# Optimization experiments

Measured on AMD Instinct MI355X. Metric: run time of the kernel, lower is better.

Reference implementation:

```python
import jax, jax.numpy as jnp
import numpy as np

N_NODES = 100000


def _gcn_conv(x, W, b, src, dst, num_nodes):
    """PyG-style GCNConv: add self-loops, symmetric normalization, linear.
    x: [N, Fin], W: [Fin, Fout], b: [Fout], src/dst: [E] (already include self-loops).
    """
    h = x @ W  # [N, Fout] transform first (PyG order), keeps edge traffic at Fout width
    ones = jnp.ones(dst.shape[0], dtype=h.dtype)
    deg = jax.ops.segment_sum(ones, dst, num_segments=num_nodes)  # degree of A+I
    dinv = jnp.where(deg > 0, jax.lax.rsqrt(deg), 0.0)
    norm = dinv[src] * dinv[dst]  # [E]
    msg = h[src] * norm[:, None]  # [E, Fout] gather + scale
    out = jax.ops.segment_sum(msg, dst, num_segments=num_nodes)  # scatter-add
    return out + b


def setup_inputs() -> dict:
    key = jax.random.key(0)
    k1, k2, k3, k4, k5 = jax.random.split(key, 5)
    input_dim, hidden_dim, embedding_dim = 128, 64, 32
    x = jax.random.normal(k1, (N_NODES, input_dim), dtype=jnp.float32)
    edge_index = jax.random.randint(k2, (2, 1600000), 0, N_NODES, dtype=jnp.int32)
    # Glorot-like init for weights
    W1 = jax.random.normal(k3, (input_dim, hidden_dim), dtype=jnp.float32) / np.sqrt(input_dim)
    b1 = jnp.zeros((hidden_dim,), dtype=jnp.float32)
    W2 = jax.random.normal(k4, (hidden_dim, embedding_dim), dtype=jnp.float32) / np.sqrt(hidden_dim)
    b2 = jnp.zeros((embedding_dim,), dtype=jnp.float32)
    return {"x": x, "edge_index": edge_index, "W1": W1, "b1": b1, "W2": W2, "b2": b2}


def reference(x, edge_index, W1, b1, W2, b2):
    num_nodes = x.shape[0]
    loop = jnp.arange(num_nodes, dtype=edge_index.dtype)
    src = jnp.concatenate([edge_index[0], loop])  # add self-loops (PyG default)
    dst = jnp.concatenate([edge_index[1], loop])
    h = _gcn_conv(x, W1, b1, src, dst, num_nodes)
    h = jax.nn.relu(h)
    z = _gcn_conv(h, W2, b2, src, dst, num_nodes)
    return z
```

## Files before the change

kernel.cpp:

```cpp
#include <hip/hip_runtime.h>
#include <hip/hip_bf16.h>


#define MAXBUCK 512

typedef unsigned int uint32;

__device__ __forceinline__ void fma4(float4& a, float s, const float4& w) {
    a.x = fmaf(s, w.x, a.x); a.y = fmaf(s, w.y, a.y);
    a.z = fmaf(s, w.z, a.z); a.w = fmaf(s, w.w, a.w);
}
__device__ __forceinline__ uint32 bf16rn(float f) {
    uint32 u = __float_as_uint(f);
    return (u + 0x7fffu + ((u >> 16) & 1u)) >> 16;
}
__device__ __forceinline__ float bflo(uint32 v) { return __uint_as_float(v << 16); }
__device__ __forceinline__ float bfhi(uint32 v) { return __uint_as_float(v & 0xffff0000u); }

__global__ void k_initcur(int* __restrict__ cursor, int nbuck, int cap) {
    int i = blockIdx.x * blockDim.x + threadIdx.x;
    if (i < nbuck) cursor[i] = i * cap;
}

__global__ __launch_bounds__(1024) void k_bin(const int* __restrict__ src,
                                              const int* __restrict__ dst, int E,
                                              int nbuck, int cap,
                                              int* __restrict__ cursor,
                                              uint32* __restrict__ pairs) {
    __shared__ int hist[MAXBUCK];
    __shared__ int base_l[MAXBUCK];
    __shared__ int cur[MAXBUCK];
    int t = threadIdx.x;
    int e0 = blockIdx.x * 4096;
    for (int i = t; i < MAXBUCK; i += 1024) { hist[i] = 0; cur[i] = 0; }
    __syncthreads();
    for (int i = t; i < 4096; i += 1024) {
        int e = e0 + i;
        if (e < E) atomicAdd(&hist[dst[e] >> 8], 1);
    }
    __syncthreads();
    for (int i = t; i < nbuck; i += 1024)
        base_l[i] = hist[i] ? atomicAdd(&cursor[i], hist[i]) : 0;
    __syncthreads();
    for (int i = t; i < 4096; i += 1024) {
        int e = e0 + i;
        if (e < E) {
            int d = dst[e];
            int b = d >> 8;
            int p = atomicAdd(&cur[b], 1);
            int idx = base_l[b] + p;
            if (idx < (b + 1) * cap)
                pairs[idx] = (uint32)src[e] | ((uint32)(d & 255) << 24);
        }
    }
}

__global__ __launch_bounds__(1024) void k_fill2(const uint32* __restrict__ pairs,
                                                const int* __restrict__ bucket_end,
                                                int cap, int N,
                                                int* __restrict__ srclist,
                                                int* __restrict__ rowstart,
                                                int* __restrict__ cnt,
                                                float* __restrict__ dinv) {
    __shared__ int hist[256];
    __shared__ int sh[256];
    __shared__ int rs_ex[256];
    __shared__ int cur[256];
    int b = blockIdx.x;
    int t = threadIdx.x;
    int start = b * cap;
    int end = min(bucket_end[b], start + cap);
    int node0 = b << 8;

    if (t < 256) { hist[t] = 0; cur[t] = 0; }
    __syncthreads();
    for (int e = start + t; e < end; e += 1024)
        atomicAdd(&hist[pairs[e] >> 24], 1);
    __syncthreads();
    int v = 0;
    if (t < 256) { v = hist[t]; sh[t] = v; }
    __syncthreads();
    for (int off = 1; off < 256; off <<= 1) {
        int tmp = 0;
        if (t < 256 && t >= off) tmp = sh[t - off];
        __syncthreads();
        if (t < 256) sh[t] += tmp;
        __syncthreads();
    }
    if (t < 256) {
        rs_ex[t] = sh[t] - v;
        int node = node0 + t;
        if (node < N) {
            rowstart[node] = start + rs_ex[t];
            cnt[node] = v;
            dinv[node] = rsqrtf((float)(v + 1));
        }
    }
    __syncthreads();
    for (int e = start + t; e < end; e += 1024) {
        uint32 pr = pairs[e];
        int dl = pr >> 24;
        int p = atomicAdd(&cur[dl], 1);
        srclist[start + rs_ex[dl] + p] = (int)(pr & 0x00FFFFFFu);
    }
}

__global__ __launch_bounds__(256) void k_gemm1(const float* __restrict__ x,
                                               const float* __restrict__ W1,
                                               const float* __restrict__ dinv,
                                               uint32* __restrict__ h1b, int n) {
    __shared__ float W1s[128 * 64];
    __shared__ float xs[32][132];
    int t = threadIdx.x;
    const float4* W1v = (const float4*)W1;
    float4* W1sv = (float4*)W1s;
    for (int i = t; i < 2048; i += 256) W1sv[i] = W1v[i];
    int node0 = blockIdx.x * 32;
    const float4* xv = (const float4*)x;
    for (int i = t; i < 1024; i += 256) {
        int nl = i >> 5, kq = i & 31;
        int node = node0 + nl;
        float4 v = make_float4(0.f, 0.f, 0.f, 0.f);
        if (node < n) v = xv[(size_t)node * 32 + kq];
        *(float4*)&xs[nl][kq * 4] = v;
    }
    __syncthreads();

    int tx = t & 15;
    int ty = t >> 4;
    int na = ty * 2, nb = na + 1;
    float4 acc0 = make_float4(0.f, 0.f, 0.f, 0.f);
    float4 acc1 = make_float4(0.f, 0.f, 0.f, 0.f);
    const float4* W1sq = (const float4*)W1s;
#pragma unroll 4
    for (int kq = 0; kq < 32; kq++) {
        float4 xa = *(const float4*)&xs[na][kq * 4];
        float4 xb = *(const float4*)&xs[nb][kq * 4];
        float4 w0 = W1sq[(kq * 4 + 0) * 16 + tx];
        float4 w1 = W1sq[(kq * 4 + 1) * 16 + tx];
        float4 w2 = W1sq[(kq * 4 + 2) * 16 + tx];
        float4 w3 = W1sq[(kq * 4 + 3) * 16 + tx];
        fma4(acc0, xa.x, w0); fma4(acc0, xa.y, w1);
        fma4(acc0, xa.z, w2); fma4(acc0, xa.w, w3);
        fma4(acc1, xb.x, w0); fma4(acc1, xb.y, w1);
        fma4(acc1, xb.z, w2); fma4(acc1, xb.w, w3);
    }
    int nA = node0 + na, nB = node0 + nb;
    if (nA < n) {
        float di = dinv[nA];
        uint2 pk = make_uint2(bf16rn(acc0.x * di) | (bf16rn(acc0.y * di) << 16),
                              bf16rn(acc0.z * di) | (bf16rn(acc0.w * di) << 16));
        ((uint2*)h1b)[(size_t)nA * 16 + tx] = pk;
    }
    if (nB < n) {
        float di = dinv[nB];
        uint2 pk = make_uint2(bf16rn(acc1.x * di) | (bf16rn(acc1.y * di) << 16),
                              bf16rn(acc1.z * di) | (bf16rn(acc1.w * di) << 16));
        ((uint2*)h1b)[(size_t)nB * 16 + tx] = pk;
    }
}

__global__ __launch_bounds__(256) void k_gather_l1(const int* __restrict__ rowstart,
                                                   const int* __restrict__ cnt,
                                                   const int* __restrict__ srclist,
                                                   const uint32* __restrict__ h1b,
                                                   const float* __restrict__ dinv,
                                                   const float* __restrict__ b1,
                                                   const float* __restrict__ W2,
                                                   unsigned short* __restrict__ h2b, int n) {
    __shared__ __align__(16) float W2s[64 * 32];
    __shared__ __align__(16) float hb[4][64];
    int t = threadIdx.x;
    {
        const float4* W2v = (const float4*)W2;
        float4* W2sv = (float4*)W2s;
        W2sv[t] = W2v[t];
        W2sv[t + 256] = W2v[t + 256];
    }
    int wid = t >> 6, lane = t & 63;
    int node = blockIdx.x * 4 + wid;
    bool valid = (node < n);
    int j = lane & 15, q = lane >> 4;

    int row = valid ? rowstart[node] : 0;
    int m_all = valid ? cnt[node] : 0;
    float di = valid ? dinv[node] : 0.0f;
    const uint2* h1v = (const uint2*)h1b;
    float a0 = 0.f, a1 = 0.f, a2 = 0.f, a3 = 0.f;
    for (int j0 = 0; j0 < m_all; j0 += 64) {
        int m = min(64, m_all - j0);
        int sidx = (lane < m) ? srclist[row + j0 + lane] : 0;
        int jj = 0;
        for (; jj + 16 <= m; jj += 16) {
            int s0 = __shfl(sidx, jj + q);
            int s1 = __shfl(sidx, jj + 4 + q);
            int s2 = __shfl(sidx, jj + 8 + q);
            int s3 = __shfl(sidx, jj + 12 + q);
            uint2 v0 = h1v[(size_t)s0 * 16 + j];
            uint2 v1 = h1v[(size_t)s1 * 16 + j];
            uint2 v2 = h1v[(size_t)s2 * 16 + j];
            uint2 v3 = h1v[(size_t)s3 * 16 + j];
            a0 += (bflo(v0.x) + bflo(v1.x)) + (bflo(v2.x) + bflo(v3.x));
            a1 += (bfhi(v0.x) + bfhi(v1.x)) + (bfhi(v2.x) + bfhi(v3.x));
            a2 += (bflo(v0.y) + bflo(v1.y)) + (bflo(v2.y) + bflo(v3.y));
            a3 += (bfhi(v0.y) + bfhi(v1.y)) + (bfhi(v2.y) + bfhi(v3.y));
        }
        for (; jj + 8 <= m; jj += 8) {
            int s0 = __shfl(sidx, jj + q);
            int s1 = __shfl(sidx, jj + 4 + q);
            uint2 v0 = h1v[(size_t)s0 * 16 + j];
            uint2 v1 = h1v[(size_t)s1 * 16 + j];
            a0 += bflo(v0.x) + bflo(v1.x);
            a1 += bfhi(v0.x) + bfhi(v1.x);
            a2 += bflo(v0.y) + bflo(v1.y);
            a3 += bfhi(v0.y) + bfhi(v1.y);
        }
        for (; jj < m; jj += 4) {
            int jidx = jj + q;
            int s = __shfl(sidx, min(jidx, m - 1));
            uint2 v = h1v[(size_t)s * 16 + j];
            if (jidx < m) {
                a0 += bflo(v.x); a1 += bfhi(v.x);
                a2 += bflo(v.y); a3 += bfhi(v.y);
            }
        }
    }
    a0 += __shfl_xor(a0, 16); a0 += __shfl_xor(a0, 32);
    a1 += __shfl_xor(a1, 16); a1 += __shfl_xor(a1, 32);
    a2 += __shfl_xor(a2, 16); a2 += __shfl_xor(a2, 32);
    a3 += __shfl_xor(a3, 16); a3 += __shfl_xor(a3, 32);
    if (valid && q == 0) {
        uint2 sv = h1v[(size_t)node * 16 + j];
        float4 bq = ((const float4*)b1)[j];
        float4 hv;
        hv.x = fmaxf((a0 + bflo(sv.x)) * di + bq.x, 0.0f);
        hv.y = fmaxf((a1 + bfhi(sv.x)) * di + bq.y, 0.0f);
        hv.z = fmaxf((a2 + bflo(sv.y)) * di + bq.z, 0.0f);
        hv.w = fmaxf((a3 + bfhi(sv.y)) * di + bq.w, 0.0f);
        *(float4*)&hb[wid][4 * j] = hv;
    }
    __syncthreads();
    if (valid) {
        int c = lane & 31, half = lane >> 5;
        int k0 = half * 32;
        float s = 0.0f;
        const float4* hb4 = (const float4*)&hb[wid][k0];
#pragma unroll
        for (int kk = 0; kk < 8; kk++) {
            float4 h4 = hb4[kk];
            int kb = k0 + kk * 4;
            s = fmaf(h4.x, W2s[(kb + 0) * 32 + c], s);
            s = fmaf(h4.y, W2s[(kb + 1) * 32 + c], s);
            s = fmaf(h4.z, W2s[(kb + 2) * 32 + c], s);
            s = fmaf(h4.w, W2s[(kb + 3) * 32 + c], s);
        }
        s += __shfl_xor(s, 32);
        if (half == 0) h2b[(size_t)node * 32 + c] = (unsigned short)bf16rn(s * di);
    }
}

__global__ __launch_bounds__(256) void k_gather_l2(const int* __restrict__ rowstart,
                                                   const int* __restrict__ cnt,
                                                   const int* __restrict__ srclist,
                                                   const uint32* __restrict__ h2b,
                                                   const float* __restrict__ dinv,
                                                   const float* __restrict__ b2v,
                                                   float* __restrict__ out, int n) {
    int t = threadIdx.x;
    int wid = t >> 6, lane = t & 63;
    int node = blockIdx.x * 4 + wid;
    if (node >= n) return;
    int j = lane & 7, o = lane >> 3;

    int row = rowstart[node], m_all = cnt[node];
    float di = dinv[node];
    const uint2* h2v = (const uint2*)h2b;
    float a0 = 0.f, a1 = 0.f, a2 = 0.f, a3 = 0.f;
    for (int j0 = 0; j0 < m_all; j0 += 64) {
        int m = min(64, m_all - j0);
        int sidx = (lane < m) ? srclist[row + j0 + lane] : 0;
        int jj = 0;
        for (; jj + 16 <= m; jj += 16) {
            int s0 = __shfl(sidx, jj + o);
            int s1 = __shfl(sidx, jj + 8 + o);
            uint2 v0 = h2v[(size_t)s0 * 8 + j];
            uint2 v1 = h2v[(size_t)s1 * 8 + j];
            a0 += bflo(v0.x) + bflo(v1.x);
            a1 += bfhi(v0.x) + bfhi(v1.x);
            a2 += bflo(v0.y) + bflo(v1.y);
            a3 += bfhi(v0.y) + bfhi(v1.y);
        }
        for (; jj + 8 <= m; jj += 8) {
            int s0 = __shfl(sidx, jj + o);
            uint2 v0 = h2v[(size_t)s0 * 8 + j];
            a0 += bflo(v0.x); a1 += bfhi(v0.x);
            a2 += bflo(v0.y); a3 += bfhi(v0.y);
        }
        if (jj < m) {
            int jidx = jj + o;
            int s = __shfl(sidx, min(jidx, m - 1));
            uint2 v = h2v[(size_t)s * 8 + j];
            if (jidx < m) {
                a0 += bflo(v.x); a1 += bfhi(v.x);
                a2 += bflo(v.y); a3 += bfhi(v.y);
            }
        }
    }
    a0 += __shfl_xor(a0, 8); a0 += __shfl_xor(a0, 16); a0 += __shfl_xor(a0, 32);
    a1 += __shfl_xor(a1, 8); a1 += __shfl_xor(a1, 16); a1 += __shfl_xor(a1, 32);
    a2 += __shfl_xor(a2, 8); a2 += __shfl_xor(a2, 16); a2 += __shfl_xor(a2, 32);
    a3 += __shfl_xor(a3, 8); a3 += __shfl_xor(a3, 16); a3 += __shfl_xor(a3, 32);
    if (o == 0) {
        float di2 = di;
        uint2 sv = h2v[(size_t)node * 8 + j];
        float4 bq = ((const float4*)b2v)[j];
        float4 ov;
        ov.x = (a0 + bflo(sv.x)) * di2 + bq.x;
        ov.y = (a1 + bfhi(sv.x)) * di2 + bq.y;
        ov.z = (a2 + bflo(sv.y)) * di2 + bq.z;
        ov.w = (a3 + bfhi(sv.y)) * di2 + bq.w;
        ((float4*)out)[(size_t)node * 8 + j] = ov;
    }
}

extern "C" void kernel_launch(void* const* d_in, const int* in_sizes, int n_in,
                              void* d_out, int out_size, void* d_ws, size_t ws_size,
                              hipStream_t stream) {
    const float* x  = (const float*)d_in[0];
    const int*   ei = (const int*)d_in[1];
    const float* W1 = (const float*)d_in[2];
    const float* b1 = (const float*)d_in[3];
    const float* W2 = (const float*)d_in[4];
    const float* b2 = (const float*)d_in[5];
    float* out = (float*)d_out;

    const int N = in_sizes[0] / 128;
    const int E = in_sizes[1] / 2;
    const int* src = ei;
    const int* dst = ei + E;
    const int nbuck = (N + 255) >> 8;

    int mean = (E + nbuck - 1) / nbuck;
    int cap = (mean + (mean >> 3) + 256 + 63) & ~63;
    size_t region = (size_t)nbuck * cap;

    char* p = (char*)d_ws;
    uint32* pairs      = (uint32*)p;    p += region * 4;
    int* srclist       = (int*)p;       p += region * 4;
    uint32* h1b        = (uint32*)p;    p += (size_t)N * 64 * 2;
    uint32* h2b        = (uint32*)p;    p += (size_t)N * 32 * 2;
    int* cursor        = (int*)p;       p += MAXBUCK * 4;
    int* rowstart      = (int*)p;       p += (size_t)N * 4;
    int* cnt           = (int*)p;       p += (size_t)N * 4;
    float* dinv        = (float*)p;     p += (size_t)N * 4;

    k_initcur<<<(nbuck + 255) / 256, 256, 0, stream>>>(cursor, nbuck, cap);
    k_bin<<<(E + 4095) / 4096, 1024, 0, stream>>>(src, dst, E, nbuck, cap, cursor, pairs);
    k_fill2<<<nbuck, 1024, 0, stream>>>(pairs, cursor, cap, N, srclist, rowstart, cnt, dinv);

    k_gemm1<<<(N + 31) / 32, 256, 0, stream>>>(x, W1, dinv, h1b, N);
    k_gather_l1<<<(N + 3) / 4, 256, 0, stream>>>(rowstart, cnt, srclist, h1b, dinv,
                                                 b1, W2, (unsigned short*)h2b, N);
    k_gather_l2<<<(N + 3) / 4, 256, 0, stream>>>(rowstart, cnt, srclist, h2b, dinv,
                                                 b2, out, N);
}
```

Baseline: 252.0 us.

## Persistent gather kernels with next-node prefetch, register W2, padded cursors

```diff
diff --git a/kernel.cpp b/kernel.cpp
--- a/kernel.cpp
+++ b/kernel.cpp
@@ -3,6 +3,7 @@
 
 
 #define MAXBUCK 512
+#define CURSTRIDE 16
 
 typedef unsigned int uint32;
 
@@ -19,7 +20,7 @@
 
 __global__ void k_initcur(int* __restrict__ cursor, int nbuck, int cap) {
     int i = blockIdx.x * blockDim.x + threadIdx.x;
-    if (i < nbuck) cursor[i] = i * cap;
+    if (i < nbuck) cursor[i * CURSTRIDE] = i * cap;
 }
 
 __global__ __launch_bounds__(1024) void k_bin(const int* __restrict__ src,
@@ -40,7 +41,7 @@
     }
     __syncthreads();
     for (int i = t; i < nbuck; i += 1024)
-        base_l[i] = hist[i] ? atomicAdd(&cursor[i], hist[i]) : 0;
+        base_l[i] = hist[i] ? atomicAdd(&cursor[i * CURSTRIDE], hist[i]) : 0;
     __syncthreads();
     for (int i = t; i < 4096; i += 1024) {
         int e = e0 + i;
@@ -69,7 +70,7 @@
     int b = blockIdx.x;
     int t = threadIdx.x;
     int start = b * cap;
-    int end = min(bucket_end[b], start + cap);
+    int end = min(bucket_end[b * CURSTRIDE], start + cap);
     int node0 = b << 8;
 
     if (t < 256) { hist[t] = 0; cur[t] = 0; }
@@ -168,94 +169,99 @@
                                                    const float* __restrict__ b1,
                                                    const float* __restrict__ W2,
                                                    unsigned short* __restrict__ h2b, int n) {
-    __shared__ __align__(16) float W2s[64 * 32];
-    __shared__ __align__(16) float hb[4][64];
-    int t = threadIdx.x;
-    {
-        const float4* W2v = (const float4*)W2;
-        float4* W2sv = (float4*)W2s;
-        W2sv[t] = W2v[t];
-        W2sv[t + 256] = W2v[t + 256];
-    }
-    int wid = t >> 6, lane = t & 63;
-    int node = blockIdx.x * 4 + wid;
-    bool valid = (node < n);
+    int t = threadIdx.x;
+    int lane = t & 63;
     int j = lane & 15, q = lane >> 4;
-
-    int row = valid ? rowstart[node] : 0;
-    int m_all = valid ? cnt[node] : 0;
-    float di = valid ? dinv[node] : 0.0f;
+    int c = lane & 31, half = lane >> 5;
+    float w2r[32];
+#pragma unroll
+    for (int kk = 0; kk < 32; kk++) w2r[kk] = W2[(half * 32 + kk) * 32 + c];
+    float4 bq = ((const float4*)b1)[j];
+
+    int nwaves = gridDim.x * 4;
+    int node = blockIdx.x * 4 + (t >> 6);
     const uint2* h1v = (const uint2*)h1b;
-    float a0 = 0.f, a1 = 0.f, a2 = 0.f, a3 = 0.f;
-    for (int j0 = 0; j0 < m_all; j0 += 64) {
-        int m = min(64, m_all - j0);
-        int sidx = (lane < m) ? srclist[row + j0 + lane] : 0;
-        int jj = 0;
-        for (; jj + 16 <= m; jj += 16) {
-            int s0 = __shfl(sidx, jj + q);
-            int s1 = __shfl(sidx, jj + 4 + q);
-            int s2 = __shfl(sidx, jj + 8 + q);
-            int s3 = __shfl(sidx, jj + 12 + q);
-            uint2 v0 = h1v[(size_t)s0 * 16 + j];
-            uint2 v1 = h1v[(size_t)s1 * 16 + j];
-            uint2 v2 = h1v[(size_t)s2 * 16 + j];
-            uint2 v3 = h1v[(size_t)s3 * 16 + j];
-            a0 += (bflo(v0.x) + bflo(v1.x)) + (bflo(v2.x) + bflo(v3.x));
-            a1 += (bfhi(v0.x) + bfhi(v1.x)) + (bfhi(v2.x) + bfhi(v3.x));
-            a2 += (bflo(v0.y) + bflo(v1.y)) + (bflo(v2.y) + bflo(v3.y));
-            a3 += (bfhi(v0.y) + bfhi(v1.y)) + (bfhi(v2.y) + bfhi(v3.y));
-        }
-        for (; jj + 8 <= m; jj += 8) {
-            int s0 = __shfl(sidx, jj + q);
-            int s1 = __shfl(sidx, jj + 4 + q);
-            uint2 v0 = h1v[(size_t)s0 * 16 + j];
-            uint2 v1 = h1v[(size_t)s1 * 16 + j];
-            a0 += bflo(v0.x) + bflo(v1.x);
-            a1 += bfhi(v0.x) + bfhi(v1.x);
-            a2 += bflo(v0.y) + bflo(v1.y);
-            a3 += bfhi(v0.y) + bfhi(v1.y);
-        }
-        for (; jj < m; jj += 4) {
-            int jidx = jj + q;
-            int s = __shfl(sidx, min(jidx, m - 1));
-            uint2 v = h1v[(size_t)s * 16 + j];
-            if (jidx < m) {
-                a0 += bflo(v.x); a1 += bfhi(v.x);
-                a2 += bflo(v.y); a3 += bfhi(v.y);
-            }
-        }
-    }
-    a0 += __shfl_xor(a0, 16); a0 += __shfl_xor(a0, 32);
-    a1 += __shfl_xor(a1, 16); a1 += __shfl_xor(a1, 32);
-    a2 += __shfl_xor(a2, 16); a2 += __shfl_xor(a2, 32);
-    a3 += __shfl_xor(a3, 16); a3 += __shfl_xor(a3, 32);
-    if (valid && q == 0) {
-        uint2 sv = h1v[(size_t)node * 16 + j];
-        float4 bq = ((const float4*)b1)[j];
-        float4 hv;
-        hv.x = fmaxf((a0 + bflo(sv.x)) * di + bq.x, 0.0f);
-        hv.y = fmaxf((a1 + bfhi(sv.x)) * di + bq.y, 0.0f);
-        hv.z = fmaxf((a2 + bflo(sv.y)) * di + bq.z, 0.0f);
-        hv.w = fmaxf((a3 + bfhi(sv.y)) * di + bq.w, 0.0f);
-        *(float4*)&hb[wid][4 * j] = hv;
-    }
-    __syncthreads();
-    if (valid) {
-        int c = lane & 31, half = lane >> 5;
-        int k0 = half * 32;
+
+    int row = 0, m_all = 0, sidx = 0;
+    float di = 0.0f;
+    uint2 sv = make_uint2(0u, 0u);
+    if (node < n) {
+        row = rowstart[node]; m_all = cnt[node]; di = dinv[node];
+        sv = h1v[(size_t)node * 16 + j];
+        sidx = (lane < m_all) ? srclist[row + lane] : 0;
+    }
+    while (node < n) {
+        int nxt = node + nwaves;
+        int row_n = 0, m_n = 0;
+        float di_n = 0.0f;
+        uint2 sv_n = make_uint2(0u, 0u);
+        if (nxt < n) {
+            row_n = rowstart[nxt]; m_n = cnt[nxt]; di_n = dinv[nxt];
+            sv_n = h1v[(size_t)nxt * 16 + j];
+        }
+        float a0 = 0.f, a1 = 0.f, a2 = 0.f, a3 = 0.f;
+        for (int j0 = 0; j0 < m_all; j0 += 64) {
+            int m = min(64, m_all - j0);
+            int sb = (j0 == 0) ? sidx : ((lane < m) ? srclist[row + j0 + lane] : 0);
+            int jj = 0;
+            for (; jj + 16 <= m; jj += 16) {
+                int s0 = __shfl(sb, jj + q);
+                int s1 = __shfl(sb, jj + 4 + q);
+                int s2 = __shfl(sb, jj + 8 + q);
+                int s3 = __shfl(sb, jj + 12 + q);
+                uint2 v0 = h1v[(size_t)s0 * 16 + j];
+                uint2 v1 = h1v[(size_t)s1 * 16 + j];
+                uint2 v2 = h1v[(size_t)s2 * 16 + j];
+                uint2 v3 = h1v[(size_t)s3 * 16 + j];
+                a0 += (bflo(v0.x) + bflo(v1.x)) + (bflo(v2.x) + bflo(v3.x));
+                a1 += (bfhi(v0.x) + bfhi(v1.x)) + (bfhi(v2.x) + bfhi(v3.x));
+                a2 += (bflo(v0.y) + bflo(v1.y)) + (bflo(v2.y) + bflo(v3.y));
+                a3 += (bfhi(v0.y) + bfhi(v1.y)) + (bfhi(v2.y) + bfhi(v3.y));
+            }
+            for (; jj + 8 <= m; jj += 8) {
+                int s0 = __shfl(sb, jj + q);
+                int s1 = __shfl(sb, jj + 4 + q);
+                uint2 v0 = h1v[(size_t)s0 * 16 + j];
+                uint2 v1 = h1v[(size_t)s1 * 16 + j];
+                a0 += bflo(v0.x) + bflo(v1.x);
+                a1 += bfhi(v0.x) + bfhi(v1.x);
+                a2 += bflo(v0.y) + bflo(v1.y);
+                a3 += bfhi(v0.y) + bfhi(v1.y);
+            }
+            for (; jj < m; jj += 4) {
+                int jidx = jj + q;
+                int s = __shfl(sb, min(jidx, m - 1));
+                uint2 v = h1v[(size_t)s * 16 + j];
+                if (jidx < m) {
+                    a0 += bflo(v.x); a1 += bfhi(v.x);
+                    a2 += bflo(v.y); a3 += bfhi(v.y);
+                }
+            }
+        }
+        int sidx_n = 0;
+        if (nxt < n) sidx_n = (lane < m_n) ? srclist[row_n + lane] : 0;
+
+        a0 += __shfl_xor(a0, 16); a0 += __shfl_xor(a0, 32);
+        a1 += __shfl_xor(a1, 16); a1 += __shfl_xor(a1, 32);
+        a2 += __shfl_xor(a2, 16); a2 += __shfl_xor(a2, 32);
+        a3 += __shfl_xor(a3, 16); a3 += __shfl_xor(a3, 32);
+        float hh0 = fmaxf((a0 + bflo(sv.x)) * di + bq.x, 0.0f);
+        float hh1 = fmaxf((a1 + bfhi(sv.x)) * di + bq.y, 0.0f);
+        float hh2 = fmaxf((a2 + bflo(sv.y)) * di + bq.z, 0.0f);
+        float hh3 = fmaxf((a3 + bfhi(sv.y)) * di + bq.w, 0.0f);
         float s = 0.0f;
-        const float4* hb4 = (const float4*)&hb[wid][k0];
 #pragma unroll
-        for (int kk = 0; kk < 8; kk++) {
-            float4 h4 = hb4[kk];
-            int kb = k0 + kk * 4;
-            s = fmaf(h4.x, W2s[(kb + 0) * 32 + c], s);
-            s = fmaf(h4.y, W2s[(kb + 1) * 32 + c], s);
-            s = fmaf(h4.z, W2s[(kb + 2) * 32 + c], s);
-            s = fmaf(h4.w, W2s[(kb + 3) * 32 + c], s);
+        for (int g = 0; g < 8; g++) {
+            int srcl = half * 8 + g;
+            s = fmaf(__shfl(hh0, srcl), w2r[4 * g + 0], s);
+            s = fmaf(__shfl(hh1, srcl), w2r[4 * g + 1], s);
+            s = fmaf(__shfl(hh2, srcl), w2r[4 * g + 2], s);
+            s = fmaf(__shfl(hh3, srcl), w2r[4 * g + 3], s);
         }
         s += __shfl_xor(s, 32);
         if (half == 0) h2b[(size_t)node * 32 + c] = (unsigned short)bf16rn(s * di);
+
+        node = nxt; row = row_n; m_all = m_n; di = di_n; sv = sv_n; sidx = sidx_n;
     }
 }
 
@@ -267,59 +273,78 @@
                                                    const float* __restrict__ b2v,
                                                    float* __restrict__ out, int n) {
     int t = threadIdx.x;
-    int wid = t >> 6, lane = t & 63;
-    int node = blockIdx.x * 4 + wid;
-    if (node >= n) return;
+    int lane = t & 63;
     int j = lane & 7, o = lane >> 3;
-
-    int row = rowstart[node], m_all = cnt[node];
-    float di = dinv[node];
+    float4 bq = ((const float4*)b2v)[j];
+
+    int nwaves = gridDim.x * 4;
+    int node = blockIdx.x * 4 + (t >> 6);
     const uint2* h2v = (const uint2*)h2b;
-    float a0 = 0.f, a1 = 0.f, a2 = 0.f, a3 = 0.f;
-    for (int j0 = 0; j0 < m_all; j0 += 64) {
-        int m = min(64, m_all - j0);
-        int sidx = (lane < m) ? srclist[row + j0 + lane] : 0;
-        int jj = 0;
-        for (; jj + 16 <= m; jj += 16) {
-            int s0 = __shfl(sidx, jj + o);
-            int s1 = __shfl(sidx, jj + 8 + o);
-            uint2 v0 = h2v[(size_t)s0 * 8 + j];
-            uint2 v1 = h2v[(size_t)s1 * 8 + j];
-            a0 += bflo(v0.x) + bflo(v1.x);
-            a1 += bfhi(v0.x) + bfhi(v1.x);
-            a2 += bflo(v0.y) + bflo(v1.y);
-            a3 += bfhi(v0.y) + bfhi(v1.y);
-        }
-        for (; jj + 8 <= m; jj += 8) {
-            int s0 = __shfl(sidx, jj + o);
-            uint2 v0 = h2v[(size_t)s0 * 8 + j];
-            a0 += bflo(v0.x); a1 += bfhi(v0.x);
-            a2 += bflo(v0.y); a3 += bfhi(v0.y);
-        }
-        if (jj < m) {
-            int jidx = jj + o;
-            int s = __shfl(sidx, min(jidx, m - 1));
-            uint2 v = h2v[(size_t)s * 8 + j];
-            if (jidx < m) {
-                a0 += bflo(v.x); a1 += bfhi(v.x);
-                a2 += bflo(v.y); a3 += bfhi(v.y);
-            }
-        }
-    }
-    a0 += __shfl_xor(a0, 8); a0 += __shfl_xor(a0, 16); a0 += __shfl_xor(a0, 32);
-    a1 += __shfl_xor(a1, 8); a1 += __shfl_xor(a1, 16); a1 += __shfl_xor(a1, 32);
-    a2 += __shfl_xor(a2, 8); a2 += __shfl_xor(a2, 16); a2 += __shfl_xor(a2, 32);
-    a3 += __shfl_xor(a3, 8); a3 += __shfl_xor(a3, 16); a3 += __shfl_xor(a3, 32);
-    if (o == 0) {
-        float di2 = di;
-        uint2 sv = h2v[(size_t)node * 8 + j];
-        float4 bq = ((const float4*)b2v)[j];
-        float4 ov;
-        ov.x = (a0 + bflo(sv.x)) * di2 + bq.x;
-        ov.y = (a1 + bfhi(sv.x)) * di2 + bq.y;
-        ov.z = (a2 + bflo(sv.y)) * di2 + bq.z;
-        ov.w = (a3 + bfhi(sv.y)) * di2 + bq.w;
-        ((float4*)out)[(size_t)node * 8 + j] = ov;
+
+    int row = 0, m_all = 0, sidx = 0;
+    float di = 0.0f;
+    uint2 sv = make_uint2(0u, 0u);
+    if (node < n) {
+        row = rowstart[node]; m_all = cnt[node]; di = dinv[node];
+        sv = h2v[(size_t)node * 8 + j];
+        sidx = (lane < m_all) ? srclist[row + lane] : 0;
+    }
+    while (node < n) {
+        int nxt = node + nwaves;
+        int row_n = 0, m_n = 0;
+        float di_n = 0.0f;
+        uint2 sv_n = make_uint2(0u, 0u);
+        if (nxt < n) {
+            row_n = rowstart[nxt]; m_n = cnt[nxt]; di_n = dinv[nxt];
+            sv_n = h2v[(size_t)nxt * 8 + j];
+        }
+        float a0 = 0.f, a1 = 0.f, a2 = 0.f, a3 = 0.f;
+        for (int j0 = 0; j0 < m_all; j0 += 64) {
+            int m = min(64, m_all - j0);
+            int sb = (j0 == 0) ? sidx : ((lane < m) ? srclist[row + j0 + lane] : 0);
+            int jj = 0;
+            for (; jj + 16 <= m; jj += 16) {
+                int s0 = __shfl(sb, jj + o);
+                int s1 = __shfl(sb, jj + 8 + o);
+                uint2 v0 = h2v[(size_t)s0 * 8 + j];
+                uint2 v1 = h2v[(size_t)s1 * 8 + j];
+                a0 += bflo(v0.x) + bflo(v1.x);
+                a1 += bfhi(v0.x) + bfhi(v1.x);
+                a2 += bflo(v0.y) + bflo(v1.y);
+                a3 += bfhi(v0.y) + bfhi(v1.y);
+            }
+            for (; jj + 8 <= m; jj += 8) {
+                int s0 = __shfl(sb, jj + o);
+                uint2 v0 = h2v[(size_t)s0 * 8 + j];
+                a0 += bflo(v0.x); a1 += bfhi(v0.x);
+                a2 += bflo(v0.y); a3 += bfhi(v0.y);
+            }
+            if (jj < m) {
+                int jidx = jj + o;
+                int s = __shfl(sb, min(jidx, m - 1));
+                uint2 v = h2v[(size_t)s * 8 + j];
+                if (jidx < m) {
+                    a0 += bflo(v.x); a1 += bfhi(v.x);
+                    a2 += bflo(v.y); a3 += bfhi(v.y);
+                }
+            }
+        }
+        int sidx_n = 0;
+        if (nxt < n) sidx_n = (lane < m_n) ? srclist[row_n + lane] : 0;
+
+        a0 += __shfl_xor(a0, 8); a0 += __shfl_xor(a0, 16); a0 += __shfl_xor(a0, 32);
+        a1 += __shfl_xor(a1, 8); a1 += __shfl_xor(a1, 16); a1 += __shfl_xor(a1, 32);
+        a2 += __shfl_xor(a2, 8); a2 += __shfl_xor(a2, 16); a2 += __shfl_xor(a2, 32);
+        a3 += __shfl_xor(a3, 8); a3 += __shfl_xor(a3, 16); a3 += __shfl_xor(a3, 32);
+        if (o == 0) {
+            float4 ov;
+            ov.x = (a0 + bflo(sv.x)) * di + bq.x;
+            ov.y = (a1 + bfhi(sv.x)) * di + bq.y;
+            ov.z = (a2 + bflo(sv.y)) * di + bq.z;
+            ov.w = (a3 + bfhi(sv.y)) * di + bq.w;
+            ((float4*)out)[(size_t)node * 8 + j] = ov;
+        }
+        node = nxt; row = row_n; m_all = m_n; di = di_n; sv = sv_n; sidx = sidx_n;
     }
 }
 
@@ -349,7 +374,7 @@
     int* srclist       = (int*)p;       p += region * 4;
     uint32* h1b        = (uint32*)p;    p += (size_t)N * 64 * 2;
     uint32* h2b        = (uint32*)p;    p += (size_t)N * 32 * 2;
-    int* cursor        = (int*)p;       p += MAXBUCK * 4;
+    int* cursor        = (int*)p;       p += MAXBUCK * CURSTRIDE * 4;
     int* rowstart      = (int*)p;       p += (size_t)N * 4;
     int* cnt           = (int*)p;       p += (size_t)N * 4;
     float* dinv        = (float*)p;     p += (size_t)N * 4;
@@ -359,8 +384,8 @@
     k_fill2<<<nbuck, 1024, 0, stream>>>(pairs, cursor, cap, N, srclist, rowstart, cnt, dinv);
 
     k_gemm1<<<(N + 31) / 32, 256, 0, stream>>>(x, W1, dinv, h1b, N);
-    k_gather_l1<<<(N + 3) / 4, 256, 0, stream>>>(rowstart, cnt, srclist, h1b, dinv,
-                                                 b1, W2, (unsigned short*)h2b, N);
-    k_gather_l2<<<(N + 3) / 4, 256, 0, stream>>>(rowstart, cnt, srclist, h2b, dinv,
-                                                 b2, out, N);
-}
+    k_gather_l1<<<1280, 256, 0, stream>>>(rowstart, cnt, srclist, h1b, dinv,
+                                          b1, W2, (unsigned short*)h2b, N);
+    k_gather_l2<<<2048, 256, 0, stream>>>(rowstart, cnt, srclist, h2b, dinv,
+                                          b2, out, N);
+}
```

After: 269.1 us. +6.8%, slower.

## Process two nodes per wavefront in gather kernels and pad bucket cursors

Applied to the files above, without the earlier changes.

```diff
diff --git a/kernel.cpp b/kernel.cpp
--- a/kernel.cpp
+++ b/kernel.cpp
@@ -3,6 +3,7 @@
 
 
 #define MAXBUCK 512
+#define CURSTRIDE 16
 
 typedef unsigned int uint32;
 
@@ -19,7 +20,7 @@
 
 __global__ void k_initcur(int* __restrict__ cursor, int nbuck, int cap) {
     int i = blockIdx.x * blockDim.x + threadIdx.x;
-    if (i < nbuck) cursor[i] = i * cap;
+    if (i < nbuck) cursor[i * CURSTRIDE] = i * cap;
 }
 
 __global__ __launch_bounds__(1024) void k_bin(const int* __restrict__ src,
@@ -40,7 +41,7 @@
     }
     __syncthreads();
     for (int i = t; i < nbuck; i += 1024)
-        base_l[i] = hist[i] ? atomicAdd(&cursor[i], hist[i]) : 0;
+        base_l[i] = hist[i] ? atomicAdd(&cursor[i * CURSTRIDE], hist[i]) : 0;
     __syncthreads();
     for (int i = t; i < 4096; i += 1024) {
         int e = e0 + i;
@@ -69,7 +70,7 @@
     int b = blockIdx.x;
     int t = threadIdx.x;
     int start = b * cap;
-    int end = min(bucket_end[b], start + cap);
+    int end = min(bucket_end[b * CURSTRIDE], start + cap);
     int node0 = b << 8;
 
     if (t < 256) { hist[t] = 0; cur[t] = 0; }
@@ -169,7 +170,7 @@
                                                    const float* __restrict__ W2,
                                                    unsigned short* __restrict__ h2b, int n) {
     __shared__ __align__(16) float W2s[64 * 32];
-    __shared__ __align__(16) float hb[4][64];
+    __shared__ __align__(16) float hb[8][64];
     int t = threadIdx.x;
     {
         const float4* W2v = (const float4*)W2;
@@ -178,73 +179,169 @@
         W2sv[t + 256] = W2v[t + 256];
     }
     int wid = t >> 6, lane = t & 63;
-    int node = blockIdx.x * 4 + wid;
-    bool valid = (node < n);
+    int nodeA = blockIdx.x * 8 + wid * 2;
+    int nodeB = nodeA + 1;
+    bool validA = (nodeA < n), validB = (nodeB < n);
     int j = lane & 15, q = lane >> 4;
 
-    int row = valid ? rowstart[node] : 0;
-    int m_all = valid ? cnt[node] : 0;
-    float di = valid ? dinv[node] : 0.0f;
+    int rowA = 0, mA = 0, rowB = 0, mB = 0;
+    float diA = 0.0f, diB = 0.0f;
+    uint2 svA = make_uint2(0u, 0u), svB = make_uint2(0u, 0u);
     const uint2* h1v = (const uint2*)h1b;
-    float a0 = 0.f, a1 = 0.f, a2 = 0.f, a3 = 0.f;
-    for (int j0 = 0; j0 < m_all; j0 += 64) {
-        int m = min(64, m_all - j0);
-        int sidx = (lane < m) ? srclist[row + j0 + lane] : 0;
+    if (validA) { rowA = rowstart[nodeA]; mA = cnt[nodeA]; diA = dinv[nodeA];
+                  svA = h1v[(size_t)nodeA * 16 + j]; }
+    if (validB) { rowB = rowstart[nodeB]; mB = cnt[nodeB]; diB = dinv[nodeB];
+                  svB = h1v[(size_t)nodeB * 16 + j]; }
+    int mA0 = min(64, mA), mB0 = min(64, mB);
+    int sidxA = (lane < mA0) ? srclist[rowA + lane] : 0;
+    int sidxB = (lane < mB0) ? srclist[rowB + lane] : 0;
+
+    float aA0 = 0.f, aA1 = 0.f, aA2 = 0.f, aA3 = 0.f;
+    float aB0 = 0.f, aB1 = 0.f, aB2 = 0.f, aB3 = 0.f;
+    int jjA = 0, jjB = 0;
+    for (; jjA + 16 <= mA0 && jjB + 16 <= mB0; jjA += 16, jjB += 16) {
+        int sA0 = __shfl(sidxA, jjA + q),      sA1 = __shfl(sidxA, jjA + 4 + q);
+        int sA2 = __shfl(sidxA, jjA + 8 + q),  sA3 = __shfl(sidxA, jjA + 12 + q);
+        int sB0 = __shfl(sidxB, jjB + q),      sB1 = __shfl(sidxB, jjB + 4 + q);
+        int sB2 = __shfl(sidxB, jjB + 8 + q),  sB3 = __shfl(sidxB, jjB + 12 + q);
+        uint2 vA0 = h1v[(size_t)sA0 * 16 + j], vA1 = h1v[(size_t)sA1 * 16 + j];
+        uint2 vA2 = h1v[(size_t)sA2 * 16 + j], vA3 = h1v[(size_t)sA3 * 16 + j];
+        uint2 vB0 = h1v[(size_t)sB0 * 16 + j], vB1 = h1v[(size_t)sB1 * 16 + j];
+        uint2 vB2 = h1v[(size_t)sB2 * 16 + j], vB3 = h1v[(size_t)sB3 * 16 + j];
+        aA0 += (bflo(vA0.x) + bflo(vA1.x)) + (bflo(vA2.x) + bflo(vA3.x));
+        aA1 += (bfhi(vA0.x) + bfhi(vA1.x)) + (bfhi(vA2.x) + bfhi(vA3.x));
+        aA2 += (bflo(vA0.y) + bflo(vA1.y)) + (bflo(vA2.y) + bflo(vA3.y));
+        aA3 += (bfhi(vA0.y) + bfhi(vA1.y)) + (bfhi(vA2.y) + bfhi(vA3.y));
+        aB0 += (bflo(vB0.x) + bflo(vB1.x)) + (bflo(vB2.x) + bflo(vB3.x));
+        aB1 += (bfhi(vB0.x) + bfhi(vB1.x)) + (bfhi(vB2.x) + bfhi(vB3.x));
+        aB2 += (bflo(vB0.y) + bflo(vB1.y)) + (bflo(vB2.y) + bflo(vB3.y));
+        aB3 += (bfhi(vB0.y) + bfhi(vB1.y)) + (bfhi(vB2.y) + bfhi(vB3.y));
+    }
+    for (; jjA + 8 <= mA0 && jjB + 8 <= mB0; jjA += 8, jjB += 8) {
+        int sA0 = __shfl(sidxA, jjA + q), sA1 = __shfl(sidxA, jjA + 4 + q);
+        int sB0 = __shfl(sidxB, jjB + q), sB1 = __shfl(sidxB, jjB + 4 + q);
+        uint2 vA0 = h1v[(size_t)sA0 * 16 + j], vA1 = h1v[(size_t)sA1 * 16 + j];
+        uint2 vB0 = h1v[(size_t)sB0 * 16 + j], vB1 = h1v[(size_t)sB1 * 16 + j];
+        aA0 += bflo(vA0.x) + bflo(vA1.x);
+        aA1 += bfhi(vA0.x) + bfhi(vA1.x);
+        aA2 += bflo(vA0.y) + bflo(vA1.y);
+        aA3 += bfhi(vA0.y) + bfhi(vA1.y);
+        aB0 += bflo(vB0.x) + bflo(vB1.x);
+        aB1 += bfhi(vB0.x) + bfhi(vB1.x);
+        aB2 += bflo(vB0.y) + bflo(vB1.y);
+        aB3 += bfhi(vB0.y) + bfhi(vB1.y);
+    }
+    for (; jjA + 8 <= mA0; jjA += 8) {
+        int s0 = __shfl(sidxA, jjA + q), s1 = __shfl(sidxA, jjA + 4 + q);
+        uint2 v0 = h1v[(size_t)s0 * 16 + j], v1 = h1v[(size_t)s1 * 16 + j];
+        aA0 += bflo(v0.x) + bflo(v1.x);
+        aA1 += bfhi(v0.x) + bfhi(v1.x);
+        aA2 += bflo(v0.y) + bflo(v1.y);
+        aA3 += bfhi(v0.y) + bfhi(v1.y);
+    }
+    for (; jjA < mA0; jjA += 4) {
+        int jidx = jjA + q;
+        int s = __shfl(sidxA, min(jidx, mA0 - 1));
+        uint2 v = h1v[(size_t)s * 16 + j];
+        if (jidx < mA0) {
+            aA0 += bflo(v.x); aA1 += bfhi(v.x);
+            aA2 += bflo(v.y); aA3 += bfhi(v.y);
+        }
+    }
+    for (; jjB + 8 <= mB0; jjB += 8) {
+        int s0 = __shfl(sidxB, jjB + q), s1 = __shfl(sidxB, jjB + 4 + q);
+        uint2 v0 = h1v[(size_t)s0 * 16 + j], v1 = h1v[(size_t)s1 * 16 + j];
+        aB0 += bflo(v0.x) + bflo(v1.x);
+        aB1 += bfhi(v0.x) + bfhi(v1.x);
+        aB2 += bflo(v0.y) + bflo(v1.y);
+        aB3 += bfhi(v0.y) + bfhi(v1.y);
+    }
+    for (; jjB < mB0; jjB += 4) {
+        int jidx = jjB + q;
+        int s = __shfl(sidxB, min(jidx, mB0 - 1));
+        uint2 v = h1v[(size_t)s * 16 + j];
+        if (jidx < mB0) {
+            aB0 += bflo(v.x); aB1 += bfhi(v.x);
+            aB2 += bflo(v.y); aB3 += bfhi(v.y);
+        }
+    }
+    for (int j0 = 64; j0 < mA; j0 += 64) {
+        int m = min(64, mA - j0);
+        int sb = (lane < m) ? srclist[rowA + j0 + lane] : 0;
         int jj = 0;
-        for (; jj + 16 <= m; jj += 16) {
-            int s0 = __shfl(sidx, jj + q);
-            int s1 = __shfl(sidx, jj + 4 + q);
-            int s2 = __shfl(sidx, jj + 8 + q);
-            int s3 = __shfl(sidx, jj + 12 + q);
-            uint2 v0 = h1v[(size_t)s0 * 16 + j];
-            uint2 v1 = h1v[(size_t)s1 * 16 + j];
-            uint2 v2 = h1v[(size_t)s2 * 16 + j];
-            uint2 v3 = h1v[(size_t)s3 * 16 + j];
-            a0 += (bflo(v0.x) + bflo(v1.x)) + (bflo(v2.x) + bflo(v3.x));
-            a1 += (bfhi(v0.x) + bfhi(v1.x)) + (bfhi(v2.x) + bfhi(v3.x));
-            a2 += (bflo(v0.y) + bflo(v1.y)) + (bflo(v2.y) + bflo(v3.y));
-            a3 += (bfhi(v0.y) + bfhi(v1.y)) + (bfhi(v2.y) + bfhi(v3.y));
-        }
         for (; jj + 8 <= m; jj += 8) {
-            int s0 = __shfl(sidx, jj + q);
-            int s1 = __shfl(sidx, jj + 4 + q);
-            uint2 v0 = h1v[(size_t)s0 * 16 + j];
-            uint2 v1 = h1v[(size_t)s1 * 16 + j];
-            a0 += bflo(v0.x) + bflo(v1.x);
-            a1 += bfhi(v0.x) + bfhi(v1.x);
-            a2 += bflo(v0.y) + bflo(v1.y);
-            a3 += bfhi(v0.y) + bfhi(v1.y);
+            int s0 = __shfl(sb, jj + q), s1 = __shfl(sb, jj + 4 + q);
+            uint2 v0 = h1v[(size_t)s0 * 16 + j], v1 = h1v[(size_t)s1 * 16 + j];
+            aA0 += bflo(v0.x) + bflo(v1.x);
+            aA1 += bfhi(v0.x) + bfhi(v1.x);
+            aA2 += bflo(v0.y) + bflo(v1.y);
+            aA3 += bfhi(v0.y) + bfhi(v1.y);
         }
         for (; jj < m; jj += 4) {
             int jidx = jj + q;
-            int s = __shfl(sidx, min(jidx, m - 1));
+            int s = __shfl(sb, min(jidx, m - 1));
             uint2 v = h1v[(size_t)s * 16 + j];
             if (jidx < m) {
-                a0 += bflo(v.x); a1 += bfhi(v.x);
-                a2 += bflo(v.y); a3 += bfhi(v.y);
+                aA0 += bflo(v.x); aA1 += bfhi(v.x);
+                aA2 += bflo(v.y); aA3 += bfhi(v.y);
             }
         }
     }
-    a0 += __shfl_xor(a0, 16); a0 += __shfl_xor(a0, 32);
-    a1 += __shfl_xor(a1, 16); a1 += __shfl_xor(a1, 32);
-    a2 += __shfl_xor(a2, 16); a2 += __shfl_xor(a2, 32);
-    a3 += __shfl_xor(a3, 16); a3 += __shfl_xor(a3, 32);
-    if (valid && q == 0) {
-        uint2 sv = h1v[(size_t)node * 16 + j];
+    for (int j0 = 64; j0 < mB; j0 += 64) {
+        int m = min(64, mB - j0);
+        int sb = (lane < m) ? srclist[rowB + j0 + lane] : 0;
+        int jj = 0;
+        for (; jj + 8 <= m; jj += 8) {
+            int s0 = __shfl(sb, jj + q), s1 = __shfl(sb, jj + 4 + q);
+            uint2 v0 = h1v[(size_t)s0 * 16 + j], v1 = h1v[(size_t)s1 * 16 + j];
+            aB0 += bflo(v0.x) + bflo(v1.x);
+            aB1 += bfhi(v0.x) + bfhi(v1.x);
+            aB2 += bflo(v0.y) + bflo(v1.y);
+            aB3 += bfhi(v0.y) + bfhi(v1.y);
+        }
+        for (; jj < m; jj += 4) {
+            int jidx = jj + q;
+            int s = __shfl(sb, min(jidx, m - 1));
+            uint2 v = h1v[(size_t)s * 16 + j];
+            if (jidx < m) {
+                aB0 += bflo(v.x); aB1 += bfhi(v.x);
+                aB2 += bflo(v.y); aB3 += bfhi(v.y);
+            }
+        }
+    }
+
+    aA0 += __shfl_xor(aA0, 16); aA0 += __shfl_xor(aA0, 32);
+    aA1 += __shfl_xor(aA1, 16); aA1 += __shfl_xor(aA1, 32);
+    aA2 += __shfl_xor(aA2, 16); aA2 += __shfl_xor(aA2, 32);
+    aA3 += __shfl_xor(aA3, 16); aA3 += __shfl_xor(aA3, 32);
+    aB0 += __shfl_xor(aB0, 16); aB0 += __shfl_xor(aB0, 32);
+    aB1 += __shfl_xor(aB1, 16); aB1 += __shfl_xor(aB1, 32);
+    aB2 += __shfl_xor(aB2, 16); aB2 += __shfl_xor(aB2, 32);
+    aB3 += __shfl_xor(aB3, 16); aB3 += __shfl_xor(aB3, 32);
+    if (validA && q == 0) {
         float4 bq = ((const float4*)b1)[j];
         float4 hv;
-        hv.x = fmaxf((a0 + bflo(sv.x)) * di + bq.x, 0.0f);
-        hv.y = fmaxf((a1 + bfhi(sv.x)) * di + bq.y, 0.0f);
-        hv.z = fmaxf((a2 + bflo(sv.y)) * di + bq.z, 0.0f);
-        hv.w = fmaxf((a3 + bfhi(sv.y)) * di + bq.w, 0.0f);
-        *(float4*)&hb[wid][4 * j] = hv;
-    }
-    __syncthreads();
-    if (valid) {
-        int c = lane & 31, half = lane >> 5;
-        int k0 = half * 32;
+        hv.x = fmaxf((aA0 + bflo(svA.x)) * diA + bq.x, 0.0f);
+        hv.y = fmaxf((aA1 + bfhi(svA.x)) * diA + bq.y, 0.0f);
+        hv.z = fmaxf((aA2 + bflo(svA.y)) * diA + bq.z, 0.0f);
+        hv.w = fmaxf((aA3 + bfhi(svA.y)) * diA + bq.w, 0.0f);
+        *(float4*)&hb[wid * 2][4 * j] = hv;
+    }
+    if (validB && q == 0) {
+        float4 bq = ((const float4*)b1)[j];
+        float4 hv;
+        hv.x = fmaxf((aB0 + bflo(svB.x)) * diB + bq.x, 0.0f);
+        hv.y = fmaxf((aB1 + bfhi(svB.x)) * diB + bq.y, 0.0f);
+        hv.z = fmaxf((aB2 + bflo(svB.y)) * diB + bq.z, 0.0f);
+        hv.w = fmaxf((aB3 + bfhi(svB.y)) * diB + bq.w, 0.0f);
+        *(float4*)&hb[wid * 2 + 1][4 * j] = hv;
+    }
+    __syncthreads();
+    int c = lane & 31, half = lane >> 5;
+    int k0 = half * 32;
+    if (validA) {
         float s = 0.0f;
-        const float4* hb4 = (const float4*)&hb[wid][k0];
+        const float4* hb4 = (const float4*)&hb[wid * 2][k0];
 #pragma unroll
         for (int kk = 0; kk < 8; kk++) {
             float4 h4 = hb4[kk];
@@ -255,7 +352,22 @@
             s = fmaf(h4.w, W2s[(kb + 3) * 32 + c], s);
         }
         s += __shfl_xor(s, 32);
-        if (half == 0) h2b[(size_t)node * 32 + c] = (unsigned short)bf16rn(s * di);
+        if (half == 0) h2b[(size_t)nodeA * 32 + c] = (unsigned short)bf16rn(s * diA);
+    }
+    if (validB) {
+        float s = 0.0f;
+        const float4* hb4 = (const float4*)&hb[wid * 2 + 1][k0];
+#pragma unroll
+        for (int kk = 0; kk < 8; kk++) {
+            float4 h4 = hb4[kk];
+            int kb = k0 + kk * 4;
+            s = fmaf(h4.x, W2s[(kb + 0) * 32 + c], s);
+            s = fmaf(h4.y, W2s[(kb + 1) * 32 + c], s);
+            s = fmaf(h4.z, W2s[(kb + 2) * 32 + c], s);
+            s = fmaf(h4.w, W2s[(kb + 3) * 32 + c], s);
+        }
+        s += __shfl_xor(s, 32);
+        if (half == 0) h2b[(size_t)nodeB * 32 + c] = (unsigned short)bf16rn(s * diB);
     }
 }
 
@@ -268,58 +380,148 @@
                                                    float* __restrict__ out, int n) {
     int t = threadIdx.x;
     int wid = t >> 6, lane = t & 63;
-    int node = blockIdx.x * 4 + wid;
-    if (node >= n) return;
+    int nodeA = blockIdx.x * 8 + wid * 2;
+    if (nodeA >= n) return;
+    int nodeB = nodeA + 1;
+    bool validB = (nodeB < n);
     int j = lane & 7, o = lane >> 3;
 
-    int row = rowstart[node], m_all = cnt[node];
-    float di = dinv[node];
+    int rowA = rowstart[nodeA], mA = cnt[nodeA];
+    float diA = dinv[nodeA];
+    int rowB = 0, mB = 0;
+    float diB = 0.0f;
     const uint2* h2v = (const uint2*)h2b;
-    float a0 = 0.f, a1 = 0.f, a2 = 0.f, a3 = 0.f;
-    for (int j0 = 0; j0 < m_all; j0 += 64) {
-        int m = min(64, m_all - j0);
-        int sidx = (lane < m) ? srclist[row + j0 + lane] : 0;
+    uint2 svA = h2v[(size_t)nodeA * 8 + j];
+    uint2 svB = make_uint2(0u, 0u);
+    if (validB) { rowB = rowstart[nodeB]; mB = cnt[nodeB]; diB = dinv[nodeB];
+                  svB = h2v[(size_t)nodeB * 8 + j]; }
+    int mA0 = min(64, mA), mB0 = min(64, mB);
+    int sidxA = (lane < mA0) ? srclist[rowA + lane] : 0;
+    int sidxB = (lane < mB0) ? srclist[rowB + lane] : 0;
+
+    float aA0 = 0.f, aA1 = 0.f, aA2 = 0.f, aA3 = 0.f;
+    float aB0 = 0.f, aB1 = 0.f, aB2 = 0.f, aB3 = 0.f;
+    int jjA = 0, jjB = 0;
+    for (; jjA + 16 <= mA0 && jjB + 16 <= mB0; jjA += 16, jjB += 16) {
+        int sA0 = __shfl(sidxA, jjA + o), sA1 = __shfl(sidxA, jjA + 8 + o);
+        int sB0 = __shfl(sidxB, jjB + o), sB1 = __shfl(sidxB, jjB + 8 + o);
+        uint2 vA0 = h2v[(size_t)sA0 * 8 + j], vA1 = h2v[(size_t)sA1 * 8 + j];
+        uint2 vB0 = h2v[(size_t)sB0 * 8 + j], vB1 = h2v[(size_t)sB1 * 8 + j];
+        aA0 += bflo(vA0.x) + bflo(vA1.x);
+        aA1 += bfhi(vA0.x) + bfhi(vA1.x);
+        aA2 += bflo(vA0.y) + bflo(vA1.y);
+        aA3 += bfhi(vA0.y) + bfhi(vA1.y);
+        aB0 += bflo(vB0.x) + bflo(vB1.x);
+        aB1 += bfhi(vB0.x) + bfhi(vB1.x);
+        aB2 += bflo(vB0.y) + bflo(vB1.y);
+        aB3 += bfhi(vB0.y) + bfhi(vB1.y);
+    }
+    for (; jjA + 8 <= mA0 && jjB + 8 <= mB0; jjA += 8, jjB += 8) {
+        int sA0 = __shfl(sidxA, jjA + o);
+        int sB0 = __shfl(sidxB, jjB + o);
+        uint2 vA0 = h2v[(size_t)sA0 * 8 + j];
+        uint2 vB0 = h2v[(size_t)sB0 * 8 + j];
+        aA0 += bflo(vA0.x); aA1 += bfhi(vA0.x);
+        aA2 += bflo(vA0.y); aA3 += bfhi(vA0.y);
+        aB0 += bflo(vB0.x); aB1 += bfhi(vB0.x);
+        aB2 += bflo(vB0.y); aB3 += bfhi(vB0.y);
+    }
+    for (; jjA + 8 <= mA0; jjA += 8) {
+        int s0 = __shfl(sidxA, jjA + o);
+        uint2 v0 = h2v[(size_t)s0 * 8 + j];
+        aA0 += bflo(v0.x); aA1 += bfhi(v0.x);
+        aA2 += bflo(v0.y); aA3 += bfhi(v0.y);
+    }
+    if (jjA < mA0) {
+        int jidx = jjA + o;
+        int s = __shfl(sidxA, min(jidx, mA0 - 1));
+        uint2 v = h2v[(size_t)s * 8 + j];
+        if (jidx < mA0) {
+            aA0 += bflo(v.x); aA1 += bfhi(v.x);
+            aA2 += bflo(v.y); aA3 += bfhi(v.y);
+        }
+    }
+    for (; jjB + 8 <= mB0; jjB += 8) {
+        int s0 = __shfl(sidxB, jjB + o);
+        uint2 v0 = h2v[(size_t)s0 * 8 + j];
+        aB0 += bflo(v0.x); aB1 += bfhi(v0.x);
+        aB2 += bflo(v0.y); aB3 += bfhi(v0.y);
+    }
+    if (jjB < mB0) {
+        int jidx = jjB + o;
+        int s = __shfl(sidxB, min(jidx, mB0 - 1));
+        uint2 v = h2v[(size_t)s * 8 + j];
+        if (jidx < mB0) {
+            aB0 += bflo(v.x); aB1 += bfhi(v.x);
+            aB2 += bflo(v.y); aB3 += bfhi(v.y);
+        }
+    }
+    for (int j0 = 64; j0 < mA; j0 += 64) {
+        int m = min(64, mA - j0);
+        int sb = (lane < m) ? srclist[rowA + j0 + lane] : 0;
         int jj = 0;
-        for (; jj + 16 <= m; jj += 16) {
-            int s0 = __shfl(sidx, jj + o);
-            int s1 = __shfl(sidx, jj + 8 + o);
+        for (; jj + 8 <= m; jj += 8) {
+            int s0 = __shfl(sb, jj + o);
             uint2 v0 = h2v[(size_t)s0 * 8 + j];
-            uint2 v1 = h2v[(size_t)s1 * 8 + j];
-            a0 += bflo(v0.x) + bflo(v1.x);
-            a1 += bfhi(v0.x) + bfhi(v1.x);
-            a2 += bflo(v0.y) + bflo(v1.y);
-            a3 += bfhi(v0.y) + bfhi(v1.y);
-        }
-        for (; jj + 8 <= m; jj += 8) {
-            int s0 = __shfl(sidx, jj + o);
-            uint2 v0 = h2v[(size_t)s0 * 8 + j];
-            a0 += bflo(v0.x); a1 += bfhi(v0.x);
-            a2 += bflo(v0.y); a3 += bfhi(v0.y);
+            aA0 += bflo(v0.x); aA1 += bfhi(v0.x);
+            aA2 += bflo(v0.y); aA3 += bfhi(v0.y);
         }
         if (jj < m) {
             int jidx = jj + o;
-            int s = __shfl(sidx, min(jidx, m - 1));
+            int s = __shfl(sb, min(jidx, m - 1));
             uint2 v = h2v[(size_t)s * 8 + j];
             if (jidx < m) {
-                a0 += bflo(v.x); a1 += bfhi(v.x);
-                a2 += bflo(v.y); a3 += bfhi(v.y);
+                aA0 += bflo(v.x); aA1 += bfhi(v.x);
+                aA2 += bflo(v.y); aA3 += bfhi(v.y);
             }
         }
     }
-    a0 += __shfl_xor(a0, 8); a0 += __shfl_xor(a0, 16); a0 += __shfl_xor(a0, 32);
-    a1 += __shfl_xor(a1, 8); a1 += __shfl_xor(a1, 16); a1 += __shfl_xor(a1, 32);
-    a2 += __shfl_xor(a2, 8); a2 += __shfl_xor(a2, 16); a2 += __shfl_xor(a2, 32);
-    a3 += __shfl_xor(a3, 8); a3 += __shfl_xor(a3, 16); a3 += __shfl_xor(a3, 32);
+    for (int j0 = 64; j0 < mB; j0 += 64) {
+        int m = min(64, mB - j0);
+        int sb = (lane < m) ? srclist[rowB + j0 + lane] : 0;
+        int jj = 0;
+        for (; jj + 8 <= m; jj += 8) {
+            int s0 = __shfl(sb, jj + o);
+            uint2 v0 = h2v[(size_t)s0 * 8 + j];
+            aB0 += bflo(v0.x); aB1 += bfhi(v0.x);
+            aB2 += bflo(v0.y); aB3 += bfhi(v0.y);
+        }
+        if (jj < m) {
+            int jidx = jj + o;
+            int s = __shfl(sb, min(jidx, m - 1));
+            uint2 v = h2v[(size_t)s * 8 + j];
+            if (jidx < m) {
+                aB0 += bflo(v.x); aB1 += bfhi(v.x);
+                aB2 += bflo(v.y); aB3 += bfhi(v.y);
+            }
+        }
+    }
+
+    a_reduce:
+    aA0 += __shfl_xor(aA0, 8); aA0 += __shfl_xor(aA0, 16); aA0 += __shfl_xor(aA0, 32);
+    aA1 += __shfl_xor(aA1, 8); aA1 += __shfl_xor(aA1, 16); aA1 += __shfl_xor(aA1, 32);
+    aA2 += __shfl_xor(aA2, 8); aA2 += __shfl_xor(aA2, 16); aA2 += __shfl_xor(aA2, 32);
+    aA3 += __shfl_xor(aA3, 8); aA3 += __shfl_xor(aA3, 16); aA3 += __shfl_xor(aA3, 32);
+    aB0 += __shfl_xor(aB0, 8); aB0 += __shfl_xor(aB0, 16); aB0 += __shfl_xor(aB0, 32);
+    aB1 += __shfl_xor(aB1, 8); aB1 += __shfl_xor(aB1, 16); aB1 += __shfl_xor(aB1, 32);
+    aB2 += __shfl_xor(aB2, 8); aB2 += __shfl_xor(aB2, 16); aB2 += __shfl_xor(aB2, 32);
+    aB3 += __shfl_xor(aB3, 8); aB3 += __shfl_xor(aB3, 16); aB3 += __shfl_xor(aB3, 32);
     if (o == 0) {
-        float di2 = di;
-        uint2 sv = h2v[(size_t)node * 8 + j];
         float4 bq = ((const float4*)b2v)[j];
         float4 ov;
-        ov.x = (a0 + bflo(sv.x)) * di2 + bq.x;
-        ov.y = (a1 + bfhi(sv.x)) * di2 + bq.y;
-        ov.z = (a2 + bflo(sv.y)) * di2 + bq.z;
-        ov.w = (a3 + bfhi(sv.y)) * di2 + bq.w;
-        ((float4*)out)[(size_t)node * 8 + j] = ov;
+        ov.x = (aA0 + bflo(svA.x)) * diA + bq.x;
+        ov.y = (aA1 + bfhi(svA.x)) * diA + bq.y;
+        ov.z = (aA2 + bflo(svA.y)) * diA + bq.z;
+        ov.w = (aA3 + bfhi(svA.y)) * diA + bq.w;
+        ((float4*)out)[(size_t)nodeA * 8 + j] = ov;
+        if (validB) {
+            float4 ob;
+            ob.x = (aB0 + bflo(svB.x)) * diB + bq.x;
+            ob.y = (aB1 + bfhi(svB.x)) * diB + bq.y;
+            ob.z = (aB2 + bflo(svB.y)) * diB + bq.z;
+            ob.w = (aB3 + bfhi(svB.y)) * diB + bq.w;
+            ((float4*)out)[(size_t)nodeB * 8 + j] = ob;
+        }
     }
 }
 
@@ -349,7 +551,7 @@
     int* srclist       = (int*)p;       p += region * 4;
     uint32* h1b        = (uint32*)p;    p += (size_t)N * 64 * 2;
     uint32* h2b        = (uint32*)p;    p += (size_t)N * 32 * 2;
-    int* cursor        = (int*)p;       p += MAXBUCK * 4;
+    int* cursor        = (int*)p;       p += MAXBUCK * CURSTRIDE * 4;
     int* rowstart      = (int*)p;       p += (size_t)N * 4;
     int* cnt           = (int*)p;       p += (size_t)N * 4;
     float* dinv        = (float*)p;     p += (size_t)N * 4;
@@ -359,8 +561,8 @@
     k_fill2<<<nbuck, 1024, 0, stream>>>(pairs, cursor, cap, N, srclist, rowstart, cnt, dinv);
 
     k_gemm1<<<(N + 31) / 32, 256, 0, stream>>>(x, W1, dinv, h1b, N);
-    k_gather_l1<<<(N + 3) / 4, 256, 0, stream>>>(rowstart, cnt, srclist, h1b, dinv,
+    k_gather_l1<<<(N + 7) / 8, 256, 0, stream>>>(rowstart, cnt, srclist, h1b, dinv,
                                                  b1, W2, (unsigned short*)h2b, N);
-    k_gather_l2<<<(N + 3) / 4, 256, 0, stream>>>(rowstart, cnt, srclist, h2b, dinv,
+    k_gather_l2<<<(N + 7) / 8, 256, 0, stream>>>(rowstart, cnt, srclist, h2b, dinv,
                                                  b2, out, N);
 }
```

New measurement: 235.7 us. -6.5%, faster.
